# Kernel optimization log

Measured on AMD Instinct MI355X. Metric: run time of the kernel, lower is better.

The kernel has to match this reference:

```python
import jax, jax.numpy as jnp
import numpy as np

N_AGENTS = 32
UNIT_DIM = 32
STATE_DIM = 1200
N_HEAD = 8
EMBED = 64
KEY_HID = 2 * EMBED
HYPER = 256
V_HID = 4 * EMBED
ATTEND_REG_COEF = 0.001
BS, T = 128, 32


def setup_inputs() -> dict:
    key = jax.random.key(0)
    ks = jax.random.split(key, 12)
    def lin(k, shape, fan_in):
        return jax.random.normal(k, shape, jnp.float32) / np.sqrt(fan_in)
    return dict(
        agent_qs=jax.random.normal(ks[0], (BS, T, N_AGENTS), jnp.float32),
        states=jax.random.normal(ks[1], (BS, T, STATE_DIM), jnp.float32),
        actions=jax.random.randint(ks[2], (BS, T, N_AGENTS), 0, 20),
        sel_W1=lin(ks[3], (N_HEAD, HYPER, STATE_DIM), STATE_DIM),
        sel_b1=jnp.zeros((N_HEAD, HYPER), jnp.float32),
        sel_W2=lin(ks[4], (N_HEAD, EMBED, HYPER), HYPER),
        key_W1=lin(ks[5], (N_HEAD, KEY_HID, UNIT_DIM + 1), UNIT_DIM + 1),
        key_b1=jnp.zeros((N_HEAD, KEY_HID), jnp.float32),
        key_W2=lin(ks[6], (N_HEAD, EMBED, KEY_HID), KEY_HID),
        wh_W1=lin(ks[7], (HYPER, STATE_DIM), STATE_DIM),
        wh_b1=jnp.zeros((HYPER,), jnp.float32),
        wh_W2=lin(ks[8], (N_HEAD, HYPER), HYPER),
        wh_b2=jnp.zeros((N_HEAD,), jnp.float32),
        v_W1=lin(ks[9], (V_HID, STATE_DIM), STATE_DIM),
        v_b1=jnp.zeros((V_HID,), jnp.float32),
        v_W2=lin(ks[10], (1, V_HID), V_HID),
        v_b2=jnp.zeros((1,), jnp.float32),
    )


def reference(agent_qs, states, actions, sel_W1, sel_b1, sel_W2, key_W1, key_b1, key_W2,
              wh_W1, wh_b1, wh_W2, wh_b2, v_W1, v_b1, v_W2, v_b2):
    bs = agent_qs.shape[0]
    s = states.reshape(-1, STATE_DIM)                       # (B, S), B = bs*T
    B = s.shape[0]
    units = s[:, :UNIT_DIM * N_AGENTS].reshape(B, N_AGENTS, UNIT_DIM)  # (B, A, U)
    q = agent_qs.reshape(B, N_AGENTS)                       # (B, A)
    # nonlinear=True: append each agent's q to its unit features
    units = jnp.concatenate([units, q[:, :, None]], axis=2)  # (B, A, U+1)
    a = actions.reshape(B, N_AGENTS)
    # selector hypernets (all heads batched): (B, H, E)
    h1 = jax.nn.relu(jnp.einsum('bs,hes->bhe', s, sel_W1) + sel_b1[None])
    sel = jnp.einsum('bhe,hde->bhd', h1, sel_W2)
    # key hypernets (all heads x all agents batched): (B, H, A, E)
    k1 = jax.nn.relu(jnp.einsum('bau,hku->bhak', units, key_W1) + key_b1[None, :, None, :])
    keys = jnp.einsum('bhak,hdk->bhad', k1, key_W2)
    logits = jnp.einsum('bhd,bhad->bha', sel, keys)          # unscaled, used for regularizer
    scaled = logits / np.sqrt(EMBED)
    scaled = jnp.where(a[:, None, :] == 0, -99999999.0, scaled)  # mask_dead
    w = jax.nn.softmax(scaled, axis=2)                       # (B, H, A)
    head_q = jnp.einsum('ba,bha->bh', q, w)                  # (B, H)
    # weighted_head + state_bias
    wh = jnp.abs(jax.nn.relu(s @ wh_W1.T + wh_b1) @ wh_W2.T + wh_b2)  # (B, H)
    v = (jax.nn.relu(s @ v_W1.T + v_b1) @ v_W2.T + v_b2)[:, 0]        # (B,)
    y = (wh * head_q).sum(axis=1) + v
    q_tot = y.reshape(bs, -1, 1)
    # sum over heads of per-head mean of squared (unscaled) logits
    attend_mag_regs = ATTEND_REG_COEF * (logits ** 2).mean(axis=(0, 2)).sum()
    # per-head entropy: sum over agents, mean over batch
    head_entropies = -(jnp.log(w + 1e-8) * w).sum(axis=2).mean(axis=0)  # (H,)
    return q_tot, attend_mag_regs, head_entropies
```

## Files before the change

kernel.cpp:

```cpp
#include <hip/hip_runtime.h>

#define B_TOT 4096
#define SDIM  1200
#define KPAD  1216
#define NA    32
#define NH    8
#define EMB   64
#define KHID  128
#define HYP   256
#define NSEL  2048
#define NTOT  2560

#define WS_H1BF 0
#define WS_MBF  (WS_H1BF + (size_t)B_TOT * NTOT / 2)
#define WS_LG   (WS_MBF  + (size_t)B_TOT * NH * KHID / 2)
#define WS_PART (WS_LG   + (size_t)B_TOT * NH * NA)
#define WS_P2   (WS_PART + (size_t)B_TOT * 16)
#define WS_ABF  (WS_P2   + (size_t)32 * 16)
#define WS_WBF  (WS_ABF  + (size_t)B_TOT * KPAD / 2)
#define WS_KW32 (WS_WBF  + (size_t)NTOT * KPAD / 2)
#define WS_W32F (WS_KW32 + (size_t)1024 * 32 / 2)
#define WS_M2T  (WS_W32F + (size_t)1024)
#define WS_UBF  (WS_M2T  + (size_t)NH * KHID * HYP / 2)

typedef __attribute__((ext_vector_type(8))) short short8v;
typedef __attribute__((ext_vector_type(4))) float floatx4;

#define GLL16(gsrc, ldst) __builtin_amdgcn_global_load_lds( \
    (const __attribute__((address_space(1))) unsigned int*)(gsrc), \
    (__attribute__((address_space(3))) unsigned int*)(ldst), 16, 0, 0)

__device__ __forceinline__ ushort f2bf(float x) {
    unsigned u = __builtin_bit_cast(unsigned, x);
    unsigned r = (u + 0x7FFFu + ((u >> 16) & 1u)) >> 16;
    return (ushort)r;
}
__device__ __forceinline__ float bf2f(ushort u) {
    unsigned x = ((unsigned)u) << 16;
    return __builtin_bit_cast(float, x);
}

__global__ __launch_bounds__(256) void k_cvt_states(
    const float* __restrict__ src, ushort* __restrict__ dst)
{
    const size_t g = (size_t)blockIdx.x * 256 + threadIdx.x;
    if (g >= (size_t)B_TOT * (KPAD / 4)) return;
    const int row = (int)(g / (KPAD / 4));
    const int c4  = (int)(g % (KPAD / 4)) * 4;
    ushort4 o = {0, 0, 0, 0};
    if (c4 < SDIM) {
        float4 v = *(const float4*)(src + (size_t)row * SDIM + c4);
        o.x = f2bf(v.x); o.y = f2bf(v.y); o.z = f2bf(v.z); o.w = f2bf(v.w);
    }
    *(ushort4*)(dst + (size_t)row * KPAD + c4) = o;
}

__global__ __launch_bounds__(256) void k_cvt_w(
    const float* __restrict__ sel_W1, const float* __restrict__ wh_W1,
    const float* __restrict__ v_W1, ushort* __restrict__ dst)
{
    const size_t g = (size_t)blockIdx.x * 256 + threadIdx.x;
    if (g >= (size_t)NTOT * (KPAD / 4)) return;
    const int row = (int)(g / (KPAD / 4));
    const int c4  = (int)(g % (KPAD / 4)) * 4;
    const float* src = (row < NSEL)       ? (sel_W1 + (size_t)row * SDIM)
                     : (row < NSEL + HYP) ? (wh_W1 + (size_t)(row - NSEL) * SDIM)
                                          : (v_W1  + (size_t)(row - NSEL - HYP) * SDIM);
    ushort4 o = {0, 0, 0, 0};
    if (c4 < SDIM) {
        float4 v = *(const float4*)(src + c4);
        o.x = f2bf(v.x); o.y = f2bf(v.y); o.z = f2bf(v.z); o.w = f2bf(v.w);
    }
    *(ushort4*)(dst + (size_t)row * KPAD + c4) = o;
}

__global__ __launch_bounds__(256) void k_cvt_units(
    const ushort* __restrict__ Abf, ushort* __restrict__ dst)
{
    const int row = blockIdx.x * 256 + threadIdx.x;
    if (row >= B_TOT * NA) return;
    const int b = row >> 5, a = row & 31;
    const ushort* s = Abf + (size_t)b * KPAD + a * 32;
    short8v v0 = *(const short8v*)(s);
    short8v v1 = *(const short8v*)(s + 8);
    short8v v2 = *(const short8v*)(s + 16);
    short8v v3 = *(const short8v*)(s + 24);
    *(short8v*)(dst + (size_t)row * 32)      = v0;
    *(short8v*)(dst + (size_t)row * 32 + 8)  = v1;
    *(short8v*)(dst + (size_t)row * 32 + 16) = v2;
    *(short8v*)(dst + (size_t)row * 32 + 24) = v3;
}

__global__ __launch_bounds__(256) void k_cvt_kw2(
    const float* __restrict__ key_W1, ushort* __restrict__ kw32,
    float* __restrict__ w32f)
{
    const int row = blockIdx.x * 256 + threadIdx.x;
    if (row >= 1024) return;
    const float* srcr = key_W1 + (size_t)row * 33;
    ushort o[32];
    #pragma unroll
    for (int u = 0; u < 32; ++u) o[u] = f2bf(srcr[u]);
    #pragma unroll
    for (int c = 0; c < 4; ++c)
        *(short8v*)(kw32 + (size_t)row * 32 + c * 8) = *(short8v*)&o[c * 8];
    w32f[row] = srcr[32];
}

__global__ __launch_bounds__(256) void k_m2(
    const float* __restrict__ sel_W2, const float* __restrict__ key_W2,
    ushort* __restrict__ M2T)
{
    __shared__ float ssel[EMB * HYP];
    __shared__ float skey[EMB][8];
    const int t  = threadIdx.x;
    const int h  = blockIdx.x;
    const int k0 = blockIdx.y * 8;

    const float4* sw = (const float4*)(sel_W2 + (size_t)h * EMB * HYP);
    #pragma unroll
    for (int j = 0; j < 16; ++j)
        ((float4*)ssel)[j * 256 + t] = sw[j * 256 + t];
    if (t < EMB) {
        #pragma unroll
        for (int kk = 0; kk < 8; ++kk)
            skey[t][kk] = key_W2[((size_t)h * EMB + t) * KHID + k0 + kk];
    }
    __syncthreads();

    const int e = t;
    float acc[8] = {};
    for (int d = 0; d < EMB; ++d) {
        const float sv = ssel[d * HYP + e];
        #pragma unroll
        for (int kk = 0; kk < 8; ++kk)
            acc[kk] = fmaf(sv, skey[d][kk], acc[kk]);
    }
    #pragma unroll
    for (int kk = 0; kk < 8; ++kk)
        M2T[((size_t)h * KHID + k0 + kk) * HYP + e] = f2bf(acc[kk]);
}

#define BK 32
__global__ __launch_bounds__(256) void k_gemm1_mfma(
    const ushort* __restrict__ Abf, const ushort* __restrict__ Wbf,
    const float* __restrict__ sel_b1, const float* __restrict__ wh_b1,
    const float* __restrict__ v_b1, ushort* __restrict__ h1bf)
{
    __shared__ ushort As[2][128 * BK];
    __shared__ ushort Bs[2][128 * BK];
    const int tid = threadIdx.x;
    const int l   = tid & 63;
    const int w   = tid >> 6;
    const int wM  = w >> 1, wN = w & 1;
    const int arow0 = blockIdx.y * 128;
    const int nrow0 = blockIdx.x * 128;

    const int srow = tid >> 2;
    const int skof = (tid & 3) * 8;
    const ushort* gA = Abf + (size_t)(arow0 + srow) * KPAD + skof;
    const ushort* gB = Wbf + (size_t)(nrow0 + srow) * KPAD + skof;

#define STAGE_G1(BUF, KK) do { \
    GLL16(gA + (KK), &As[BUF][srow * BK + skof]); \
    GLL16(gA + (size_t)64 * KPAD + (KK), &As[BUF][(64 + srow) * BK + skof]); \
    GLL16(gB + (KK), &Bs[BUF][srow * BK + skof]); \
    GLL16(gB + (size_t)64 * KPAD + (KK), &Bs[BUF][(64 + srow) * BK + skof]); \
} while (0)

    floatx4 acc[4][4] = {};

    STAGE_G1(0, 0);
    __syncthreads();
    int cur = 0;
    for (int k0 = 0; k0 < KPAD; k0 += BK) {
        if (k0 + BK < KPAD) STAGE_G1(cur ^ 1, k0 + BK);

        const int kch = (l >> 4) * 8;
        short8v av[4], bv[4];
        #pragma unroll
        for (int mi = 0; mi < 4; ++mi)
            av[mi] = *(const short8v*)&As[cur][(wM * 64 + mi * 16 + (l & 15)) * BK + kch];
        #pragma unroll
        for (int ni = 0; ni < 4; ++ni)
            bv[ni] = *(const short8v*)&Bs[cur][(wN * 64 + ni * 16 + (l & 15)) * BK + kch];
        #pragma unroll
        for (int mi = 0; mi < 4; ++mi)
            #pragma unroll
            for (int ni = 0; ni < 4; ++ni)
                acc[mi][ni] = __builtin_amdgcn_mfma_f32_16x16x32_bf16(
                    av[mi], bv[ni], acc[mi][ni], 0, 0, 0);
        __syncthreads();
        cur ^= 1;
    }

    float bias_n[4];
    #pragma unroll
    for (int ni = 0; ni < 4; ++ni) {
        const int col = nrow0 + wN * 64 + ni * 16 + (l & 15);
        bias_n[ni] = (col < NSEL)       ? sel_b1[col]
                   : (col < NSEL + HYP) ? wh_b1[col - NSEL]
                                        : v_b1[col - NSEL - HYP];
    }
    #pragma unroll
    for (int mi = 0; mi < 4; ++mi) {
        const int row = arow0 + wM * 64 + mi * 16 + (l >> 4) * 4;
        #pragma unroll
        for (int ni = 0; ni < 4; ++ni) {
            const int col = nrow0 + wN * 64 + ni * 16 + (l & 15);
            #pragma unroll
            for (int r = 0; r < 4; ++r)
                h1bf[(size_t)(row + r) * NTOT + col] =
                    f2bf(fmaxf(acc[mi][ni][r] + bias_n[ni], 0.f));
        }
    }
}

__global__ __launch_bounds__(256) void k_m_mfma(
    const ushort* __restrict__ h1bf, const ushort* __restrict__ M2T,
    ushort* __restrict__ m_out)
{
    __shared__ ushort As[2][64 * BK];
    __shared__ ushort Bs[2][128 * BK];
    const int tid = threadIdx.x;
    const int l   = tid & 63;
    const int w   = tid >> 6;
    const int wM  = w >> 1, wN = w & 1;
    const int h     = blockIdx.x;
    const int brow0 = blockIdx.y * 64;

    const int srow = tid >> 2;
    const int skof = (tid & 3) * 8;
    const ushort* gA = h1bf + (size_t)(brow0 + srow) * NTOT + h * HYP + skof;
    const ushort* gB = M2T + ((size_t)h * KHID + srow) * HYP + skof;

#define STAGE_M(BUF, KK) do { \
    GLL16(gA + (KK), &As[BUF][srow * BK + skof]); \
    GLL16(gB + (KK), &Bs[BUF][srow * BK + skof]); \
    GLL16(gB + (size_t)64 * HYP + (KK), &Bs[BUF][(64 + srow) * BK + skof]); \
} while (0)

    floatx4 acc[2][4] = {};

    STAGE_M(0, 0);
    __syncthreads();
    int cur = 0;
    for (int k0 = 0; k0 < HYP; k0 += BK) {
        if (k0 + BK < HYP) STAGE_M(cur ^ 1, k0 + BK);

        const int kch = (l >> 4) * 8;
        short8v av[2], bv[4];
        #pragma unroll
        for (int mi = 0; mi < 2; ++mi)
            av[mi] = *(const short8v*)&As[cur][(wM * 32 + mi * 16 + (l & 15)) * BK + kch];
        #pragma unroll
        for (int ni = 0; ni < 4; ++ni)
            bv[ni] = *(const short8v*)&Bs[cur][(wN * 64 + ni * 16 + (l & 15)) * BK + kch];
        #pragma unroll
        for (int mi = 0; mi < 2; ++mi)
            #pragma unroll
            for (int ni = 0; ni < 4; ++ni)
                acc[mi][ni] = __builtin_amdgcn_mfma_f32_16x16x32_bf16(
                    av[mi], bv[ni], acc[mi][ni], 0, 0, 0);
        __syncthreads();
        cur ^= 1;
    }

    #pragma unroll
    for (int mi = 0; mi < 2; ++mi) {
        const int row = brow0 + wM * 32 + mi * 16 + (l >> 4) * 4;
        #pragma unroll
        for (int ni = 0; ni < 4; ++ni) {
            const int col = wN * 64 + ni * 16 + (l & 15);
            #pragma unroll
            for (int r = 0; r < 4; ++r)
                m_out[((size_t)(row + r) * NH + h) * KHID + col] =
                    f2bf(acc[mi][ni][r]);
        }
    }
}

__global__ __launch_bounds__(256) void k_logits_mfma(
    const ushort* __restrict__ Ubf, const ushort* __restrict__ KW32,
    const float* __restrict__ W32f, const float* __restrict__ key_b1,
    const float* __restrict__ agent_qs, const ushort* __restrict__ m_in,
    float* __restrict__ logits)
{
    const int tid = threadIdx.x;
    const int l   = tid & 63;
    const int w   = tid >> 6;
    const int b   = blockIdx.x * 4 + w;
    const int urow0 = b * NA;

    short8v av[2];
    float4 qv[2];
    #pragma unroll
    for (int mi = 0; mi < 2; ++mi) {
        av[mi] = *(const short8v*)(
            Ubf + (size_t)(urow0 + mi * 16 + (l & 15)) * 32 + (l >> 4) * 8);
        qv[mi] = *(const float4*)(
            agent_qs + (size_t)b * NA + mi * 16 + (l >> 4) * 4);
    }

    for (int h = 0; h < NH; ++h) {
        short8v bv[8];
        float b1r[8], w32r[8], mr[8];
        #pragma unroll
        for (int ni = 0; ni < 8; ++ni) {
            const int k = ni * 16 + (l & 15);
            bv[ni]   = *(const short8v*)(
                KW32 + ((size_t)h * KHID + k) * 32 + (l >> 4) * 8);
            b1r[ni]  = key_b1[h * KHID + k];
            w32r[ni] = W32f[h * KHID + k];
            mr[ni]   = bf2f(m_in[((size_t)b * NH + h) * KHID + k]);
        }
        floatx4 acc[2][8] = {};
        #pragma unroll
        for (int mi = 0; mi < 2; ++mi)
            #pragma unroll
            for (int ni = 0; ni < 8; ++ni)
                acc[mi][ni] = __builtin_amdgcn_mfma_f32_16x16x32_bf16(
                    av[mi], bv[ni], acc[mi][ni], 0, 0, 0);

        #pragma unroll
        for (int mi = 0; mi < 2; ++mi) {
            float s0 = 0.f, s1 = 0.f, s2 = 0.f, s3 = 0.f;
            #pragma unroll
            for (int ni = 0; ni < 8; ++ni) {
                const float b1v = b1r[ni], wv = w32r[ni], mv = mr[ni];
                s0 = fmaf(fmaxf(fmaf(qv[mi].x, wv, acc[mi][ni][0] + b1v), 0.f), mv, s0);
                s1 = fmaf(fmaxf(fmaf(qv[mi].y, wv, acc[mi][ni][1] + b1v), 0.f), mv, s1);
                s2 = fmaf(fmaxf(fmaf(qv[mi].z, wv, acc[mi][ni][2] + b1v), 0.f), mv, s2);
                s3 = fmaf(fmaxf(fmaf(qv[mi].w, wv, acc[mi][ni][3] + b1v), 0.f), mv, s3);
            }
            #pragma unroll
            for (int off = 8; off >= 1; off >>= 1) {
                s0 += __shfl_xor(s0, off);
                s1 += __shfl_xor(s1, off);
                s2 += __shfl_xor(s2, off);
                s3 += __shfl_xor(s3, off);
            }
            if ((l & 15) == 0) {
                float4 o = {s0, s1, s2, s3};
                *(float4*)(logits + ((size_t)b * NH + h) * NA
                           + mi * 16 + (l >> 4) * 4) = o;
            }
        }
    }
}

__global__ __launch_bounds__(256) void k_softmax(
    const float* __restrict__ logits, const float* __restrict__ agent_qs,
    const int* __restrict__ actions, const ushort* __restrict__ h1bf,
    const float* __restrict__ wh_W2, const float* __restrict__ wh_b2,
    const float* __restrict__ v_W2, const float* __restrict__ v_b2,
    float* __restrict__ out, float* __restrict__ part)
{
    __shared__ float qs[NA];
    __shared__ int   act_s[NA];
    __shared__ float whs[NH];
    __shared__ float hq[NH];
    __shared__ float vred[4];
    const int b = blockIdx.x, t = threadIdx.x;
    if (t < NA) {
        qs[t]    = agent_qs[(size_t)b * NA + t];
        act_s[t] = actions[(size_t)b * NA + t];
    }
    const int h = t >> 5, a = t & 31;
    {
        float acc = 0.f;
        #pragma unroll
        for (int j = 0; j < 8; ++j) {
            const int e = a + 32 * j;
            acc = fmaf(bf2f(h1bf[(size_t)b * NTOT + NSEL + e]),
                       wh_W2[h * HYP + e], acc);
        }
        #pragma unroll
        for (int off = 16; off >= 1; off >>= 1) acc += __shfl_xor(acc, off, 32);
        if (a == 0) whs[h] = fabsf(acc + wh_b2[h]);
    }
    {
        float acc = bf2f(h1bf[(size_t)b * NTOT + NSEL + HYP + t]) * v_W2[t];
        #pragma unroll
        for (int off = 32; off >= 1; off >>= 1) acc += __shfl_xor(acc, off);
        if ((t & 63) == 0) vred[t >> 6] = acc;
    }
    __syncthreads();

    const float lg = logits[((size_t)b * NH + h) * NA + a];
    float sc = (act_s[a] == 0) ? -99999999.0f : lg * 0.125f;

    float mx = sc;
    #pragma unroll
    for (int off = 16; off >= 1; off >>= 1) mx = fmaxf(mx, __shfl_xor(mx, off, 32));
    const float e = expf(sc - mx);
    float sum = e;
    #pragma unroll
    for (int off = 16; off >= 1; off >>= 1) sum += __shfl_xor(sum, off, 32);
    const float wgt = e / sum;

    float r_sq  = lg * lg;
    float r_hq  = qs[a] * wgt;
    float r_ent = -wgt * logf(wgt + 1e-8f);
    #pragma unroll
    for (int off = 16; off >= 1; off >>= 1) {
        r_sq  += __shfl_xor(r_sq,  off, 32);
        r_hq  += __shfl_xor(r_hq,  off, 32);
        r_ent += __shfl_xor(r_ent, off, 32);
    }
    if (a == 0) {
        hq[h] = r_hq;
        part[(size_t)b * 16 + h]     = r_sq;
        part[(size_t)b * 16 + 8 + h] = r_ent;
    }
    __syncthreads();
    if (t == 0) {
        float y = vred[0] + vred[1] + vred[2] + vred[3] + v_b2[0];
        #pragma unroll
        for (int i = 0; i < NH; ++i) y = fmaf(whs[i], hq[i], y);
        out[b] = y;
    }
}

__global__ __launch_bounds__(256) void k_final_s1(
    const float* __restrict__ part, float* __restrict__ part2)
{
    __shared__ float red[16][17];
    const int t = threadIdx.x;
    const int c = t & 15, rl = t >> 4;
    const int rbase = blockIdx.x * 128 + rl;
    float v0 = 0.f, v1 = 0.f, v2 = 0.f, v3 = 0.f;
    #pragma unroll
    for (int j = 0; j < 8; j += 4) {
        v0 += part[(size_t)(rbase + (j + 0) * 16) * 16 + c];
        v1 += part[(size_t)(rbase + (j + 1) * 16) * 16 + c];
        v2 += part[(size_t)(rbase + (j + 2) * 16) * 16 + c];
        v3 += part[(size_t)(rbase + (j + 3) * 16) * 16 + c];
    }
    red[rl][c] = (v0 + v1) + (v2 + v3);
    __syncthreads();
    if (t < 16) {
        float s = 0.f;
        #pragma unroll
        for (int i = 0; i < 16; ++i) s += red[i][t];
        part2[blockIdx.x * 16 + t] = s;
    }
}

__global__ __launch_bounds__(256) void k_final_s2(
    const float* __restrict__ part2, float* __restrict__ out)
{
    __shared__ float red[16][17];
    __shared__ float tot[16];
    const int t = threadIdx.x;
    {
        const int g = t >> 4, c = t & 15;
        red[g][c] = part2[t] + part2[t + 256];
    }
    __syncthreads();
    if (t < 16) {
        float s = 0.f;
        #pragma unroll
        for (int i = 0; i < 16; ++i) s += red[i][t];
        tot[t] = s;
    }
    __syncthreads();
    if (t == 0) {
        float s = 0.f;
        #pragma unroll
        for (int i = 0; i < 8; ++i) s += tot[i];
        out[B_TOT] = 0.001f * (s / (float)((size_t)B_TOT * NA));
    }
    if (t >= 8 && t < 16)
        out[B_TOT + 1 + (t - 8)] = tot[t] / (float)B_TOT;
}

extern "C" void kernel_launch(void* const* d_in, const int* in_sizes, int n_in,
                              void* d_out, int out_size, void* d_ws, size_t ws_size,
                              hipStream_t stream) {
    (void)in_sizes; (void)n_in; (void)out_size; (void)ws_size;
    const float* agent_qs = (const float*)d_in[0];
    const float* states   = (const float*)d_in[1];
    const int*   actions  = (const int*)d_in[2];
    const float* sel_W1   = (const float*)d_in[3];
    const float* sel_b1   = (const float*)d_in[4];
    const float* sel_W2   = (const float*)d_in[5];
    const float* key_W1   = (const float*)d_in[6];
    const float* key_b1   = (const float*)d_in[7];
    const float* key_W2   = (const float*)d_in[8];
    const float* wh_W1    = (const float*)d_in[9];
    const float* wh_b1    = (const float*)d_in[10];
    const float* wh_W2    = (const float*)d_in[11];
    const float* wh_b2    = (const float*)d_in[12];
    const float* v_W1     = (const float*)d_in[13];
    const float* v_b1     = (const float*)d_in[14];
    const float* v_W2     = (const float*)d_in[15];
    const float* v_b2     = (const float*)d_in[16];

    float* out = (float*)d_out;
    float* ws  = (float*)d_ws;
    ushort* h1bf  = (ushort*)(ws + WS_H1BF);
    ushort* m_buf = (ushort*)(ws + WS_MBF);
    float* lg_buf = ws + WS_LG;
    float* part   = ws + WS_PART;
    float* part2  = ws + WS_P2;
    ushort* Abf   = (ushort*)(ws + WS_ABF);
    ushort* Wbf   = (ushort*)(ws + WS_WBF);
    ushort* KW32  = (ushort*)(ws + WS_KW32);
    float*  W32f  = ws + WS_W32F;
    ushort* M2T   = (ushort*)(ws + WS_M2T);
    ushort* Ubf   = (ushort*)(ws + WS_UBF);

    {
        const int groups_a = B_TOT * (KPAD / 4);
        const int groups_w = NTOT * (KPAD / 4);
        k_cvt_states<<<(groups_a + 255) / 256, 256, 0, stream>>>(states, Abf);
        k_cvt_w<<<(groups_w + 255) / 256, 256, 0, stream>>>(sel_W1, wh_W1, v_W1, Wbf);
        k_cvt_kw2<<<4, 256, 0, stream>>>(key_W1, KW32, W32f);
        k_cvt_units<<<(B_TOT * NA + 255) / 256, 256, 0, stream>>>(Abf, Ubf);
        k_m2<<<dim3(NH, KHID / 8), 256, 0, stream>>>(sel_W2, key_W2, M2T);
    }
    k_gemm1_mfma<<<dim3(NTOT / 128, B_TOT / 128), 256, 0, stream>>>(
        Abf, Wbf, sel_b1, wh_b1, v_b1, h1bf);
    k_m_mfma<<<dim3(NH, B_TOT / 64), 256, 0, stream>>>(h1bf, M2T, m_buf);
    k_logits_mfma<<<dim3(B_TOT / 4), 256, 0, stream>>>(
        Ubf, KW32, W32f, key_b1, agent_qs, m_buf, lg_buf);
    k_softmax<<<dim3(B_TOT), 256, 0, stream>>>(
        lg_buf, agent_qs, actions, h1bf, wh_W2, wh_b2, v_W2, v_b2, out, part);
    k_final_s1<<<32, 256, 0, stream>>>(part, part2);
    k_final_s2<<<1, 256, 0, stream>>>(part2, out);
}
```

Baseline: 123.7 us.

## Drop units copy kernel and retile gemm1 with BK=64 swizzled LDS

Removes the k_cvt_units kernel and has the logits kernel read unit features straight from the bf16 states buffer, which saves one launch and a copy pass. The main GEMM moves from a double-buffered BK=32 loop to a single-buffered BK=64 tile with an XOR-swizzled LDS layout, so there are half as many barrier iterations and fewer LDS bank conflicts. Dropping double buffering means global loads no longer overlap with the MFMA work, so each iteration now stalls on its load.

```diff
diff --git a/kernel.cpp b/kernel.cpp
--- a/kernel.cpp
+++ b/kernel.cpp
@@ -21,7 +21,6 @@
 #define WS_KW32 (WS_WBF  + (size_t)NTOT * KPAD / 2)
 #define WS_W32F (WS_KW32 + (size_t)1024 * 32 / 2)
 #define WS_M2T  (WS_W32F + (size_t)1024)
-#define WS_UBF  (WS_M2T  + (size_t)NH * KHID * HYP / 2)
 
 typedef __attribute__((ext_vector_type(8))) short short8v;
 typedef __attribute__((ext_vector_type(4))) float floatx4;
@@ -74,23 +73,6 @@
     *(ushort4*)(dst + (size_t)row * KPAD + c4) = o;
 }
 
-__global__ __launch_bounds__(256) void k_cvt_units(
-    const ushort* __restrict__ Abf, ushort* __restrict__ dst)
-{
-    const int row = blockIdx.x * 256 + threadIdx.x;
-    if (row >= B_TOT * NA) return;
-    const int b = row >> 5, a = row & 31;
-    const ushort* s = Abf + (size_t)b * KPAD + a * 32;
-    short8v v0 = *(const short8v*)(s);
-    short8v v1 = *(const short8v*)(s + 8);
-    short8v v2 = *(const short8v*)(s + 16);
-    short8v v3 = *(const short8v*)(s + 24);
-    *(short8v*)(dst + (size_t)row * 32)      = v0;
-    *(short8v*)(dst + (size_t)row * 32 + 8)  = v1;
-    *(short8v*)(dst + (size_t)row * 32 + 16) = v2;
-    *(short8v*)(dst + (size_t)row * 32 + 24) = v3;
-}
-
 __global__ __launch_bounds__(256) void k_cvt_kw2(
     const float* __restrict__ key_W1, ushort* __restrict__ kw32,
     float* __restrict__ w32f)
@@ -141,14 +123,14 @@
         M2T[((size_t)h * KHID + k0 + kk) * HYP + e] = f2bf(acc[kk]);
 }
 
-#define BK 32
+#define BKG 64
 __global__ __launch_bounds__(256) void k_gemm1_mfma(
     const ushort* __restrict__ Abf, const ushort* __restrict__ Wbf,
     const float* __restrict__ sel_b1, const float* __restrict__ wh_b1,
     const float* __restrict__ v_b1, ushort* __restrict__ h1bf)
 {
-    __shared__ ushort As[2][128 * BK];
-    __shared__ ushort Bs[2][128 * BK];
+    __shared__ ushort As[128 * BKG];
+    __shared__ ushort Bs[128 * BKG];
     const int tid = threadIdx.x;
     const int l   = tid & 63;
     const int w   = tid >> 6;
@@ -156,42 +138,46 @@
     const int arow0 = blockIdx.y * 128;
     const int nrow0 = blockIdx.x * 128;
 
-    const int srow = tid >> 2;
-    const int skof = (tid & 3) * 8;
-    const ushort* gA = Abf + (size_t)(arow0 + srow) * KPAD + skof;
-    const ushort* gB = Wbf + (size_t)(nrow0 + srow) * KPAD + skof;
-
-#define STAGE_G1(BUF, KK) do { \
-    GLL16(gA + (KK), &As[BUF][srow * BK + skof]); \
-    GLL16(gA + (size_t)64 * KPAD + (KK), &As[BUF][(64 + srow) * BK + skof]); \
-    GLL16(gB + (KK), &Bs[BUF][srow * BK + skof]); \
-    GLL16(gB + (size_t)64 * KPAD + (KK), &Bs[BUF][(64 + srow) * BK + skof]); \
-} while (0)
+    const int srow   = tid >> 3;
+    const int schunk = tid & 7;
+    const int scol   = (schunk ^ (srow & 7)) * 8;
+    const ushort* gA = Abf + (size_t)(arow0 + srow) * KPAD + scol;
+    const ushort* gB = Wbf + (size_t)(nrow0 + srow) * KPAD + scol;
+    ushort* lA = &As[tid * 8];
+    ushort* lB = &Bs[tid * 8];
 
     floatx4 acc[4][4] = {};
 
-    STAGE_G1(0, 0);
-    __syncthreads();
-    int cur = 0;
-    for (int k0 = 0; k0 < KPAD; k0 += BK) {
-        if (k0 + BK < KPAD) STAGE_G1(cur ^ 1, k0 + BK);
-
-        const int kch = (l >> 4) * 8;
-        short8v av[4], bv[4];
-        #pragma unroll
-        for (int mi = 0; mi < 4; ++mi)
-            av[mi] = *(const short8v*)&As[cur][(wM * 64 + mi * 16 + (l & 15)) * BK + kch];
-        #pragma unroll
-        for (int ni = 0; ni < 4; ++ni)
-            bv[ni] = *(const short8v*)&Bs[cur][(wN * 64 + ni * 16 + (l & 15)) * BK + kch];
-        #pragma unroll
-        for (int mi = 0; mi < 4; ++mi)
-            #pragma unroll
-            for (int ni = 0; ni < 4; ++ni)
-                acc[mi][ni] = __builtin_amdgcn_mfma_f32_16x16x32_bf16(
-                    av[mi], bv[ni], acc[mi][ni], 0, 0, 0);
+    for (int k0 = 0; k0 < KPAD; k0 += BKG) {
+        #pragma unroll
+        for (int c = 0; c < 4; ++c) {
+            GLL16(gA + (size_t)(c * 32) * KPAD + k0, lA + c * 2048);
+            GLL16(gB + (size_t)(c * 32) * KPAD + k0, lB + c * 2048);
+        }
         __syncthreads();
-        cur ^= 1;
+
+        #pragma unroll
+        for (int kk = 0; kk < 2; ++kk) {
+            const int ch = kk * 4 + (l >> 4);
+            short8v av[4], bv[4];
+            #pragma unroll
+            for (int mi = 0; mi < 4; ++mi) {
+                const int row = wM * 64 + mi * 16 + (l & 15);
+                av[mi] = *(const short8v*)&As[row * BKG + (ch ^ (row & 7)) * 8];
+            }
+            #pragma unroll
+            for (int ni = 0; ni < 4; ++ni) {
+                const int row = wN * 64 + ni * 16 + (l & 15);
+                bv[ni] = *(const short8v*)&Bs[row * BKG + (ch ^ (row & 7)) * 8];
+            }
+            #pragma unroll
+            for (int mi = 0; mi < 4; ++mi)
+                #pragma unroll
+                for (int ni = 0; ni < 4; ++ni)
+                    acc[mi][ni] = __builtin_amdgcn_mfma_f32_16x16x32_bf16(
+                        av[mi], bv[ni], acc[mi][ni], 0, 0, 0);
+        }
+        __syncthreads();
     }
 
     float bias_n[4];
@@ -216,6 +202,7 @@
     }
 }
 
+#define BK 32
 __global__ __launch_bounds__(256) void k_m_mfma(
     const ushort* __restrict__ h1bf, const ushort* __restrict__ M2T,
     ushort* __restrict__ m_out)
@@ -281,7 +268,7 @@
 }
 
 __global__ __launch_bounds__(256) void k_logits_mfma(
-    const ushort* __restrict__ Ubf, const ushort* __restrict__ KW32,
+    const ushort* __restrict__ Abf, const ushort* __restrict__ KW32,
     const float* __restrict__ W32f, const float* __restrict__ key_b1,
     const float* __restrict__ agent_qs, const ushort* __restrict__ m_in,
     float* __restrict__ logits)
@@ -290,14 +277,14 @@
     const int l   = tid & 63;
     const int w   = tid >> 6;
     const int b   = blockIdx.x * 4 + w;
-    const int urow0 = b * NA;
 
     short8v av[2];
     float4 qv[2];
     #pragma unroll
     for (int mi = 0; mi < 2; ++mi) {
+        const int a = mi * 16 + (l & 15);
         av[mi] = *(const short8v*)(
-            Ubf + (size_t)(urow0 + mi * 16 + (l & 15)) * 32 + (l >> 4) * 8);
+            Abf + (size_t)b * KPAD + a * 32 + (l >> 4) * 8);
         qv[mi] = *(const float4*)(
             agent_qs + (size_t)b * NA + mi * 16 + (l >> 4) * 4);
     }
@@ -509,7 +496,6 @@
     ushort* KW32  = (ushort*)(ws + WS_KW32);
     float*  W32f  = ws + WS_W32F;
     ushort* M2T   = (ushort*)(ws + WS_M2T);
-    ushort* Ubf   = (ushort*)(ws + WS_UBF);
 
     {
         const int groups_a = B_TOT * (KPAD / 4);
@@ -517,14 +503,13 @@
         k_cvt_states<<<(groups_a + 255) / 256, 256, 0, stream>>>(states, Abf);
         k_cvt_w<<<(groups_w + 255) / 256, 256, 0, stream>>>(sel_W1, wh_W1, v_W1, Wbf);
         k_cvt_kw2<<<4, 256, 0, stream>>>(key_W1, KW32, W32f);
-        k_cvt_units<<<(B_TOT * NA + 255) / 256, 256, 0, stream>>>(Abf, Ubf);
         k_m2<<<dim3(NH, KHID / 8), 256, 0, stream>>>(sel_W2, key_W2, M2T);
     }
     k_gemm1_mfma<<<dim3(NTOT / 128, B_TOT / 128), 256, 0, stream>>>(
         Abf, Wbf, sel_b1, wh_b1, v_b1, h1bf);
     k_m_mfma<<<dim3(NH, B_TOT / 64), 256, 0, stream>>>(h1bf, M2T, m_buf);
     k_logits_mfma<<<dim3(B_TOT / 4), 256, 0, stream>>>(
-        Ubf, KW32, W32f, key_b1, agent_qs, m_buf, lg_buf);
+        Abf, KW32, W32f, key_b1, agent_qs, m_buf, lg_buf);
     k_softmax<<<dim3(B_TOT), 256, 0, stream>>>(
         lg_buf, agent_qs, actions, h1bf, wh_W2, wh_b2, v_W2, v_b2, out, part);
     k_final_s1<<<32, 256, 0, stream>>>(part, part2);
```

Result: faster. 116.0 us (-6.3%).
